# Kernel optimization log

Hardware: AMD Instinct MI355X
Metric: run time of the kernel (lower is better)

## Reference

```python
import jax, jax.numpy as jnp
import numpy as np


def setup_inputs() -> dict:
    key = jax.random.key(0)
    k1, k2 = jax.random.split(key)
    # positive inputs -> positive matmul outputs, so log is well-defined
    x = jax.random.uniform(k1, (8, 2048, 1024), dtype=jnp.float32)
    matrix = jax.random.uniform(k2, (1024, 1024), dtype=jnp.float32)
    return {"x": x, "matrix": matrix}


def reference(x, matrix):
    # mm_big: shifted quantized matmul; mm_small: no-shift quantized matmul.
    # In float math both compute the same product (quantization differs only
    # in fixed-point scaling), so we compute it once; XLA would CSE anyway.
    y_big = jnp.einsum('bsk,km->bsm', x, matrix)    # [B,S,M]
    y_small = jnp.einsum('bsk,km->bsm', x, matrix)  # NoShiftMM, same float math

    big = (y_big > 0).astype(x.dtype)   # gt0
    small = 1.0 - big                   # oplus(neg(big)) = 1 + (-big)

    eps = jnp.finfo(x.dtype).tiny
    # AddIdentityTLUT(torch.log): LUT approximation of log; float reference is log.
    z_big = jnp.log(jnp.maximum(y_big, eps)) * big      # lut_big -> mul_big
    z_small = jnp.log(jnp.maximum(y_small, eps)) * small  # lut_small -> mul_small
    return z_big + z_small  # add_output
```

## Files before the change

### kernel.cpp

```cpp
#include <hip/hip_runtime.h>
#include <cstdint>
#include <cstddef>

#define M_GLOB 16384
#define N_GLOB 1024
#define K_GLOB 1024

#define BM 128
#define BN 128
#define BKF 128

typedef unsigned char  u8;
typedef unsigned short u16;
typedef __attribute__((ext_vector_type(4))) float  f32x4;
typedef __attribute__((ext_vector_type(4))) unsigned int  u32x4;
typedef __attribute__((ext_vector_type(2))) unsigned int  u32x2;
typedef __attribute__((ext_vector_type(8))) __bf16 bf16x8;

typedef const __attribute__((address_space(1))) void* gas1_t;
typedef __attribute__((address_space(3))) void* las3_t;

static __device__ __forceinline__ void load_lds16(const void* g, void* l) {
    __builtin_amdgcn_global_load_lds((gas1_t)g, (las3_t)l, 16, 0, 0);
}

static __device__ __forceinline__ unsigned rne2_bf16(float lo, float hi) {
    unsigned a = __builtin_bit_cast(unsigned, lo);
    unsigned b = __builtin_bit_cast(unsigned, hi);
    a += 0x7FFFu + ((a >> 16) & 1u);
    b += 0x7FFFu + ((b >> 16) & 1u);
    return (a >> 16) | (b & 0xFFFF0000u);
}

static __device__ __forceinline__ unsigned pack2_bf16(float lo, float hi) {
    unsigned bl = __builtin_bit_cast(unsigned, lo);
    unsigned bh = __builtin_bit_cast(unsigned, hi);
    return (bh & 0xFFFF0000u) | (bl >> 16);
}

static __device__ __forceinline__ unsigned cvt4_fp8(float a, float b, float c, float d) {
    int w = __builtin_amdgcn_cvt_pk_fp8_f32(a, b, 0, false);
    w = __builtin_amdgcn_cvt_pk_fp8_f32(c, d, w, true);
    return (unsigned)w;
}

__global__ __launch_bounds__(256)
void prep_fp8_kernel(const float* __restrict__ A, u8* __restrict__ Ab,
                     const float* __restrict__ B, u8* __restrict__ Bt, int nA) {
    __shared__ float tile[32][33];
    const int tid = threadIdx.x;
    if ((int)blockIdx.x < nA) {
        const size_t i = ((size_t)blockIdx.x * 256 + tid) * 16;
        f32x4 f0 = *(const f32x4*)(A + i);
        f32x4 f1 = *(const f32x4*)(A + i + 4);
        f32x4 f2 = *(const f32x4*)(A + i + 8);
        f32x4 f3 = *(const f32x4*)(A + i + 12);
        u32x4 o;
        o.x = cvt4_fp8(f0.x, f0.y, f0.z, f0.w);
        o.y = cvt4_fp8(f1.x, f1.y, f1.z, f1.w);
        o.z = cvt4_fp8(f2.x, f2.y, f2.z, f2.w);
        o.w = cvt4_fp8(f3.x, f3.y, f3.z, f3.w);
        *(u32x4*)(Ab + i) = o;
    } else {
        const int bid = (int)blockIdx.x - nA;
        const int n0 = (bid & 31) * 32;
        const int k0 = (bid >> 5) * 32;
        const int tx = tid & 31;
        const int ty = tid >> 5;
#pragma unroll
        for (int i = 0; i < 32; i += 8)
            tile[ty + i][tx] = B[(size_t)(k0 + ty + i) * N_GLOB + n0 + tx];
        __syncthreads();
#pragma unroll
        for (int i = 0; i < 32; i += 8) {
            int w = __builtin_amdgcn_cvt_pk_fp8_f32(tile[tx][ty + i], 0.f, 0, false);
            Bt[(size_t)(n0 + ty + i) * K_GLOB + k0 + tx] = (u8)(w & 0xFF);
        }
    }
}

__global__ __launch_bounds__(256)
void gemm_fp8_kernel(const u8* __restrict__ A,
                     const u8* __restrict__ Bt,
                     float* __restrict__ C)
{
    __shared__ __attribute__((aligned(16))) char smem[33792];
    float* Cs = (float*)smem;

    const int tid  = threadIdx.x;
    const int wave = tid >> 6;
    const int lane = tid & 63;
    const int wr   = wave >> 1;
    const int wc   = wave & 1;
    const int quad = lane >> 4;
    const int l16  = lane & 15;

    const int b    = blockIdx.x;
    const int xcd  = b & 7;
    const int idx  = b >> 3;
    const int m0   = (xcd * 16 + (idx >> 3)) * BM;
    const int n0   = (idx & 7) * BN;

    const int srow = lane >> 3;
    const int sc   = (lane & 7) ^ srow;
    const u8* gA = A  + (size_t)(m0 + srow) * K_GLOB + sc * 16;
    const u8* gB = Bt + (size_t)(n0 + srow) * K_GLOB + sc * 16;

    f32x4 acc[4][4];
#pragma unroll
    for (int i = 0; i < 4; ++i)
#pragma unroll
        for (int j = 0; j < 4; ++j)
            acc[i][j] = f32x4{0.f, 0.f, 0.f, 0.f};

    const int swz = l16 & 7;
    const int qh  = quad >> 1;
    const int qo  = (quad & 1) * 8;

    for (int kt = 0; kt < K_GLOB / BKF; ++kt) {
        const size_t k0 = (size_t)kt * BKF;
#pragma unroll
        for (int s = 0; s < 4; ++s) {
            const int rows0 = (s * 4 + wave) * 8;
            load_lds16(gA + (size_t)rows0 * K_GLOB + k0, smem + rows0 * 128);
            load_lds16(gB + (size_t)rows0 * K_GLOB + k0, smem + 16384 + rows0 * 128);
        }
        __syncthreads();

#pragma unroll
        for (int kk = 0; kk < 4; ++kk) {
            const int p = ((kk * 2 + qh) ^ swz) * 16 + qo;
            long af[4], bfr[4];
#pragma unroll
            for (int i = 0; i < 4; ++i) {
                const int row = wr * 64 + i * 16 + l16;
                af[i] = __builtin_bit_cast(long, *(const u32x2*)(smem + row * 128 + p));
            }
#pragma unroll
            for (int j = 0; j < 4; ++j) {
                const int row = wc * 64 + j * 16 + l16;
                bfr[j] = __builtin_bit_cast(long, *(const u32x2*)(smem + 16384 + row * 128 + p));
            }
#pragma unroll
            for (int i = 0; i < 4; ++i)
#pragma unroll
                for (int j = 0; j < 4; ++j)
                    acc[i][j] = __builtin_amdgcn_mfma_f32_16x16x32_fp8_fp8(af[i], bfr[j], acc[i][j], 0, 0, 0);
        }
        __syncthreads();
    }

    const float LN2 = 0.69314718055994530942f;
    const int c4 = tid & 31;
    const int r0 = tid >> 5;
#pragma unroll
    for (int h = 0; h < 2; ++h) {
        __syncthreads();
        if (wr == h) {
#pragma unroll
            for (int i = 0; i < 4; ++i)
#pragma unroll
                for (int j = 0; j < 4; ++j) {
                    const int col = wc * 64 + j * 16 + l16;
#pragma unroll
                    for (int r = 0; r < 4; ++r) {
                        const int row = i * 16 + quad * 4 + r;
                        float v = fmaxf(acc[i][j][r], 1.17549435e-38f);
                        Cs[row * 132 + col] = __log2f(v) * LN2;
                    }
                }
        }
        __syncthreads();
#pragma unroll
        for (int s = 0; s < 8; ++s) {
            const int row = s * 8 + r0;
            f32x4 v = *(const f32x4*)&Cs[row * 132 + c4 * 4];
            __builtin_nontemporal_store(v,
                (f32x4*)&C[(size_t)(m0 + h * 64 + row) * N_GLOB + n0 + c4 * 4]);
        }
    }
}

#define LDK 40
template <bool BT_READY>
__global__ __launch_bounds__(256)
void logmm_fused_kernel(const float* __restrict__ A,
                        const u16*   __restrict__ Btb,
                        const float* __restrict__ Bf,
                        float* __restrict__ C)
{
    __shared__ u16 As[BM][LDK];
    __shared__ u16 Bs[BN][LDK];

    const int tid  = threadIdx.x;
    const int wave = tid >> 6;
    const int lane = tid & 63;
    const int wr   = wave >> 1;
    const int wc   = wave & 1;
    const int quad = lane >> 4;
    const int l16  = lane & 15;

    const int m0 = blockIdx.y * BM;
    const int n0 = blockIdx.x * BN;

    f32x4 acc[4][4];
#pragma unroll
    for (int i = 0; i < 4; ++i)
#pragma unroll
        for (int j = 0; j < 4; ++j)
            acc[i][j] = f32x4{0.f, 0.f, 0.f, 0.f};

    const int ga_row = tid >> 2;
    const int ga_c8  = (tid & 3) * 8;
    const int fb_nt = tid >> 3;
    const int fb_kt = tid & 7;

    for (int kt = 0; kt < K_GLOB / 32; ++kt) {
        const int k0 = kt * 32;
#pragma unroll
        for (int s = 0; s < 2; ++s) {
            const int row = ga_row + s * 64;
            const float* src = A + (size_t)(m0 + row) * K_GLOB + k0 + ga_c8;
            f32x4 f0 = *(const f32x4*)src;
            f32x4 f1 = *(const f32x4*)(src + 4);
            u32x4 o;
            o.x = pack2_bf16(f0.x, f0.y);
            o.y = pack2_bf16(f0.z, f0.w);
            o.z = pack2_bf16(f1.x, f1.y);
            o.w = pack2_bf16(f1.z, f1.w);
            *(u32x4*)&As[row][ga_c8] = o;
        }
        if (BT_READY) {
#pragma unroll
            for (int s = 0; s < 2; ++s) {
                const int row = ga_row + s * 64;
                u32x4 v = *(const u32x4*)(Btb + (size_t)(n0 + row) * K_GLOB + k0 + ga_c8);
                *(u32x4*)&Bs[row][ga_c8] = v;
            }
        } else {
            f32x4 r0 = *(const f32x4*)(Bf + (size_t)(k0 + fb_kt * 4 + 0) * N_GLOB + n0 + fb_nt * 4);
            f32x4 r1 = *(const f32x4*)(Bf + (size_t)(k0 + fb_kt * 4 + 1) * N_GLOB + n0 + fb_nt * 4);
            f32x4 r2 = *(const f32x4*)(Bf + (size_t)(k0 + fb_kt * 4 + 2) * N_GLOB + n0 + fb_nt * 4);
            f32x4 r3 = *(const f32x4*)(Bf + (size_t)(k0 + fb_kt * 4 + 3) * N_GLOB + n0 + fb_nt * 4);
#pragma unroll
            for (int j = 0; j < 4; ++j) {
                u32x2 o;
                o.x = pack2_bf16(r0[j], r1[j]);
                o.y = pack2_bf16(r2[j], r3[j]);
                *(u32x2*)&Bs[fb_nt * 4 + j][fb_kt * 4] = o;
            }
        }

        __syncthreads();

        bf16x8 af[4], bfr[4];
#pragma unroll
        for (int i = 0; i < 4; ++i)
            af[i] = __builtin_bit_cast(bf16x8, *(const u32x4*)&As[wr * 64 + i * 16 + l16][quad * 8]);
#pragma unroll
        for (int j = 0; j < 4; ++j)
            bfr[j] = __builtin_bit_cast(bf16x8, *(const u32x4*)&Bs[wc * 64 + j * 16 + l16][quad * 8]);

#pragma unroll
        for (int i = 0; i < 4; ++i)
#pragma unroll
            for (int j = 0; j < 4; ++j)
                acc[i][j] = __builtin_amdgcn_mfma_f32_16x16x32_bf16(af[i], bfr[j], acc[i][j], 0, 0, 0);

        __syncthreads();
    }

    const float LN2 = 0.69314718055994530942f;
#pragma unroll
    for (int i = 0; i < 4; ++i) {
#pragma unroll
        for (int j = 0; j < 4; ++j) {
            const int col = n0 + wc * 64 + j * 16 + l16;
#pragma unroll
            for (int r = 0; r < 4; ++r) {
                const int row = m0 + wr * 64 + i * 16 + quad * 4 + r;
                float v = fmaxf(acc[i][j][r], 1.17549435e-38f);
                C[(size_t)row * N_GLOB + col] = __log2f(v) * LN2;
            }
        }
    }
}

extern "C" void kernel_launch(void* const* d_in, const int* in_sizes, int n_in,
                              void* d_out, int out_size, void* d_ws, size_t ws_size,
                              hipStream_t stream) {
    const float* A = (const float*)d_in[0];
    const float* B = (const float*)d_in[1];
    float* C = (float*)d_out;

    const size_t bt_bytes = (size_t)N_GLOB * K_GLOB;
    const size_t ab_bytes = (size_t)M_GLOB * K_GLOB;
    const int nA = (M_GLOB * K_GLOB) / (256 * 16);

    if (ws_size >= bt_bytes + ab_bytes) {
        u8* Bt = (u8*)d_ws;
        u8* Ab = (u8*)d_ws + bt_bytes;
        prep_fp8_kernel<<<nA + 1024, 256, 0, stream>>>(A, Ab, B, Bt, nA);
        gemm_fp8_kernel<<<(M_GLOB / BM) * (N_GLOB / BN), 256, 0, stream>>>(Ab, Bt, C);
    } else {
        logmm_fused_kernel<false><<<dim3(N_GLOB / BN, M_GLOB / BM), 256, 0, stream>>>(A, nullptr, B, C);
    }
}
```

Baseline: 141.6 us.

## Switch FP8 GEMM to MI355 scaled 32x32x64 MFMA with unit scales

Replaces the 16x16x32 fp8 MFMA inner loop with the gfx950 scaled 32x32x64 f8f6f4 MFMA, using identity exponent scales (0x7F). Operand fragments are now read from swizzled LDS as two 16-byte loads per row, and the accumulator layout plus the log epilogue are remapped to the 32x32 output layout, written in four 32-row passes. It also trims LDS to 32 KB and adds a launch bound of 4 blocks per SM to raise occupancy. The bigger MFMA does more work per instruction and needs fewer LDS reads, at the cost of register pressure from the 16-wide accumulators. Unused fallback template code is removed.

```diff
diff --git a/kernel.cpp b/kernel.cpp
--- a/kernel.cpp
+++ b/kernel.cpp
@@ -13,8 +13,10 @@
 typedef unsigned char  u8;
 typedef unsigned short u16;
 typedef __attribute__((ext_vector_type(4))) float  f32x4;
+typedef __attribute__((ext_vector_type(16))) float f32x16;
 typedef __attribute__((ext_vector_type(4))) unsigned int  u32x4;
 typedef __attribute__((ext_vector_type(2))) unsigned int  u32x2;
+typedef __attribute__((ext_vector_type(8))) int  i32x8;
 typedef __attribute__((ext_vector_type(8))) __bf16 bf16x8;
 
 typedef const __attribute__((address_space(1))) void* gas1_t;
@@ -22,14 +24,6 @@
 
 static __device__ __forceinline__ void load_lds16(const void* g, void* l) {
     __builtin_amdgcn_global_load_lds((gas1_t)g, (las3_t)l, 16, 0, 0);
-}
-
-static __device__ __forceinline__ unsigned rne2_bf16(float lo, float hi) {
-    unsigned a = __builtin_bit_cast(unsigned, lo);
-    unsigned b = __builtin_bit_cast(unsigned, hi);
-    a += 0x7FFFu + ((a >> 16) & 1u);
-    b += 0x7FFFu + ((b >> 16) & 1u);
-    return (a >> 16) | (b & 0xFFFF0000u);
 }
 
 static __device__ __forceinline__ unsigned pack2_bf16(float lo, float hi) {
@@ -79,12 +73,12 @@
     }
 }
 
-__global__ __launch_bounds__(256)
-void gemm_fp8_kernel(const u8* __restrict__ A,
-                     const u8* __restrict__ Bt,
-                     float* __restrict__ C)
+__global__ __launch_bounds__(256, 4)
+void gemm_mx_kernel(const u8* __restrict__ A,
+                    const u8* __restrict__ Bt,
+                    float* __restrict__ C)
 {
-    __shared__ __attribute__((aligned(16))) char smem[33792];
+    __shared__ __attribute__((aligned(16))) char smem[32768];
     float* Cs = (float*)smem;
 
     const int tid  = threadIdx.x;
@@ -92,8 +86,8 @@
     const int lane = tid & 63;
     const int wr   = wave >> 1;
     const int wc   = wave & 1;
-    const int quad = lane >> 4;
-    const int l16  = lane & 15;
+    const int l32  = lane & 31;
+    const int half = lane >> 5;
 
     const int b    = blockIdx.x;
     const int xcd  = b & 7;
@@ -106,16 +100,17 @@
     const u8* gA = A  + (size_t)(m0 + srow) * K_GLOB + sc * 16;
     const u8* gB = Bt + (size_t)(n0 + srow) * K_GLOB + sc * 16;
 
-    f32x4 acc[4][4];
-#pragma unroll
-    for (int i = 0; i < 4; ++i)
-#pragma unroll
-        for (int j = 0; j < 4; ++j)
-            acc[i][j] = f32x4{0.f, 0.f, 0.f, 0.f};
-
-    const int swz = l16 & 7;
-    const int qh  = quad >> 1;
-    const int qo  = (quad & 1) * 8;
+    f32x16 acc[2][2];
+#pragma unroll
+    for (int i = 0; i < 2; ++i)
+#pragma unroll
+        for (int j = 0; j < 2; ++j)
+#pragma unroll
+            for (int r = 0; r < 16; ++r)
+                acc[i][j][r] = 0.f;
+
+    const int swz = lane & 7;
+    const int scale1 = 0x7F7F7F7F;
 
     for (int kt = 0; kt < K_GLOB / BKF; ++kt) {
         const size_t k0 = (size_t)kt * BKF;
@@ -128,24 +123,35 @@
         __syncthreads();
 
 #pragma unroll
-        for (int kk = 0; kk < 4; ++kk) {
-            const int p = ((kk * 2 + qh) ^ swz) * 16 + qo;
-            long af[4], bfr[4];
-#pragma unroll
-            for (int i = 0; i < 4; ++i) {
-                const int row = wr * 64 + i * 16 + l16;
-                af[i] = __builtin_bit_cast(long, *(const u32x2*)(smem + row * 128 + p));
-            }
-#pragma unroll
-            for (int j = 0; j < 4; ++j) {
-                const int row = wc * 64 + j * 16 + l16;
-                bfr[j] = __builtin_bit_cast(long, *(const u32x2*)(smem + 16384 + row * 128 + p));
-            }
-#pragma unroll
-            for (int i = 0; i < 4; ++i)
-#pragma unroll
-                for (int j = 0; j < 4; ++j)
-                    acc[i][j] = __builtin_amdgcn_mfma_f32_16x16x32_fp8_fp8(af[i], bfr[j], acc[i][j], 0, 0, 0);
+        for (int s = 0; s < 2; ++s) {
+            const int c0 = s * 4 + half * 2;
+            const int p0 = ((c0    ) ^ swz) * 16;
+            const int p1 = ((c0 + 1) ^ swz) * 16;
+            i32x8 af[2], bf[2];
+#pragma unroll
+            for (int i = 0; i < 2; ++i) {
+                const int row = wr * 64 + i * 32 + l32;
+                u32x4 lo = *(const u32x4*)(smem + row * 128 + p0);
+                u32x4 hi = *(const u32x4*)(smem + row * 128 + p1);
+                af[i][0] = lo.x; af[i][1] = lo.y; af[i][2] = lo.z; af[i][3] = lo.w;
+                af[i][4] = hi.x; af[i][5] = hi.y; af[i][6] = hi.z; af[i][7] = hi.w;
+            }
+#pragma unroll
+            for (int j = 0; j < 2; ++j) {
+                const int row = wc * 64 + j * 32 + l32;
+                u32x4 lo = *(const u32x4*)(smem + 16384 + row * 128 + p0);
+                u32x4 hi = *(const u32x4*)(smem + 16384 + row * 128 + p1);
+                bf[j][0] = lo.x; bf[j][1] = lo.y; bf[j][2] = lo.z; bf[j][3] = lo.w;
+                bf[j][4] = hi.x; bf[j][5] = hi.y; bf[j][6] = hi.z; bf[j][7] = hi.w;
+            }
+#pragma unroll
+            for (int i = 0; i < 2; ++i)
+#pragma unroll
+                for (int j = 0; j < 2; ++j)
+                    acc[i][j] = __builtin_amdgcn_mfma_scale_f32_32x32x64_f8f6f4(
+                        af[i], bf[j], acc[i][j],
+                        0 , 0 ,
+                        0, scale1, 0, scale1);
         }
         __syncthreads();
     }
@@ -154,38 +160,35 @@
     const int c4 = tid & 31;
     const int r0 = tid >> 5;
 #pragma unroll
-    for (int h = 0; h < 2; ++h) {
-        __syncthreads();
-        if (wr == h) {
-#pragma unroll
-            for (int i = 0; i < 4; ++i)
-#pragma unroll
-                for (int j = 0; j < 4; ++j) {
-                    const int col = wc * 64 + j * 16 + l16;
-#pragma unroll
-                    for (int r = 0; r < 4; ++r) {
-                        const int row = i * 16 + quad * 4 + r;
-                        float v = fmaxf(acc[i][j][r], 1.17549435e-38f);
-                        Cs[row * 132 + col] = __log2f(v) * LN2;
-                    }
+    for (int q = 0; q < 4; ++q) {
+        __syncthreads();
+        if (wr == (q >> 1)) {
+            const int i = q & 1;
+#pragma unroll
+            for (int j = 0; j < 2; ++j) {
+                const int col = wc * 64 + j * 32 + l32;
+#pragma unroll
+                for (int r = 0; r < 16; ++r) {
+                    const int row = (r & 3) + 8 * (r >> 2) + 4 * half;
+                    float v = fmaxf(acc[i][j][r], 1.17549435e-38f);
+                    Cs[row * 132 + col] = __log2f(v) * LN2;
                 }
-        }
-        __syncthreads();
-#pragma unroll
-        for (int s = 0; s < 8; ++s) {
-            const int row = s * 8 + r0;
+            }
+        }
+        __syncthreads();
+#pragma unroll
+        for (int s2 = 0; s2 < 4; ++s2) {
+            const int row = s2 * 8 + r0;
             f32x4 v = *(const f32x4*)&Cs[row * 132 + c4 * 4];
             __builtin_nontemporal_store(v,
-                (f32x4*)&C[(size_t)(m0 + h * 64 + row) * N_GLOB + n0 + c4 * 4]);
+                (f32x4*)&C[(size_t)(m0 + q * 32 + row) * N_GLOB + n0 + c4 * 4]);
         }
     }
 }
 
 #define LDK 40
-template <bool BT_READY>
 __global__ __launch_bounds__(256)
 void logmm_fused_kernel(const float* __restrict__ A,
-                        const u16*   __restrict__ Btb,
                         const float* __restrict__ Bf,
                         float* __restrict__ C)
 {
@@ -193,8 +196,8 @@
     __shared__ u16 Bs[BN][LDK];
 
     const int tid  = threadIdx.x;
+    const int lane = tid & 63;
     const int wave = tid >> 6;
-    const int lane = tid & 63;
     const int wr   = wave >> 1;
     const int wc   = wave & 1;
     const int quad = lane >> 4;
@@ -230,14 +233,7 @@
             o.w = pack2_bf16(f1.z, f1.w);
             *(u32x4*)&As[row][ga_c8] = o;
         }
-        if (BT_READY) {
-#pragma unroll
-            for (int s = 0; s < 2; ++s) {
-                const int row = ga_row + s * 64;
-                u32x4 v = *(const u32x4*)(Btb + (size_t)(n0 + row) * K_GLOB + k0 + ga_c8);
-                *(u32x4*)&Bs[row][ga_c8] = v;
-            }
-        } else {
+        {
             f32x4 r0 = *(const f32x4*)(Bf + (size_t)(k0 + fb_kt * 4 + 0) * N_GLOB + n0 + fb_nt * 4);
             f32x4 r1 = *(const f32x4*)(Bf + (size_t)(k0 + fb_kt * 4 + 1) * N_GLOB + n0 + fb_nt * 4);
             f32x4 r2 = *(const f32x4*)(Bf + (size_t)(k0 + fb_kt * 4 + 2) * N_GLOB + n0 + fb_nt * 4);
@@ -301,8 +297,8 @@
         u8* Bt = (u8*)d_ws;
         u8* Ab = (u8*)d_ws + bt_bytes;
         prep_fp8_kernel<<<nA + 1024, 256, 0, stream>>>(A, Ab, B, Bt, nA);
-        gemm_fp8_kernel<<<(M_GLOB / BM) * (N_GLOB / BN), 256, 0, stream>>>(Ab, Bt, C);
+        gemm_mx_kernel<<<(M_GLOB / BM) * (N_GLOB / BN), 256, 0, stream>>>(Ab, Bt, C);
     } else {
-        logmm_fused_kernel<false><<<dim3(N_GLOB / BN, M_GLOB / BM), 256, 0, stream>>>(A, nullptr, B, C);
-    }
-}
+        logmm_fused_kernel<<<dim3(N_GLOB / BN, M_GLOB / BM), 256, 0, stream>>>(A, B, C);
+    }
+}
```

Result: faster. 138.0 us (-2.6%).
